# Optimization experiments

Hardware: AMD Instinct MI355X
Metric: run time of the kernel (lower is better)

Reference implementation:

```python
import jax, jax.numpy as jnp
import numpy as np

K = 16          # neighbors per query (args.k)
EPS_NORM = 1e-5  # LayerNorm / BatchNorm eps (torch default)


def _knn_edges(xyz, B, n):
    # batch-aware kNN: equal-sized batches, edges never cross batch boundary
    x = xyz.reshape(B, n, 3)
    d2 = jnp.sum((x[:, :, None, :] - x[:, None, :, :]) ** 2, -1)   # [B,n,n]
    _, idx = jax.lax.top_k(-d2, K)                                 # [B,n,K] local neighbor ids
    col = (idx + (jnp.arange(B) * n)[:, None, None]).reshape(-1)   # source (neighbor) [E]
    row = jnp.repeat(jnp.arange(B * n), K)                         # target (query)    [E]
    return row, col


def _forward(support_xyz, batch_index, features, lang_features, mask_flattened,
             W1, b1, ln_g, ln_b, W2, b2,
             Wl1, bl1, bn_g, bn_b, Wl2, bl2,
             Wr1, br1, Wr2, br2, row, col):
    N = support_xyz.shape[0]
    B, L, Fl = lang_features.shape
    # feat_encoder: Linear -> LayerNorm -> ReLU -> Linear
    h = features @ W1 + b1
    mu = h.mean(-1, keepdims=True)
    var = ((h - mu) ** 2).mean(-1, keepdims=True)
    h = (h - mu) / jnp.sqrt(var + EPS_NORM) * ln_g + ln_b
    feats = jax.nn.relu(h) @ W2 + b2                               # [N,F]
    # lang_encoder: Linear -> BatchNorm1d (batch statistics) -> ReLU -> Linear
    hl = lang_features.reshape(B * L, Fl) @ Wl1 + bl1
    mul = hl.mean(0)
    varl = ((hl - mul) ** 2).mean(0)
    hl = (hl - mul) / jnp.sqrt(varl + EPS_NORM) * bn_g + bn_b
    lang = (jax.nn.relu(hl) @ Wl2 + bl2).reshape(B, L, -1)         # [B,L,F]
    lang_flat = lang[batch_index]                                  # [N,L,F]
    # per-point / per-token attention logits
    atten = jnp.einsum('nf,nlf->nl', feats, lang_flat)             # [N,L]
    # segment softmax over incoming kNN edges (CenterOp max / add)
    attenmax = jax.ops.segment_max(atten[col], row, num_segments=N, indices_are_sorted=True)
    a = jnp.exp(atten[col] - attenmax[row])                        # [E,L]
    attensum = jax.ops.segment_sum(a, row, num_segments=N, indices_are_sorted=True)
    # CenterConv message
    att = a / attensum[row] * mask_flattened[row]                  # [E,L]
    att = att / (att.sum(-1, keepdims=True) + 1e-7)
    ctx = jnp.einsum('el,elf->ef', att, lang_flat[col])            # [E,F] attended lang feat
    xi, xj = support_xyz[row], support_xyz[col]
    d = xi - xj
    nrm = jnp.sqrt(jnp.sum(d * d, -1, keepdims=True) + 1e-12)
    ew = jnp.concatenate([xi, xj, d, nrm], -1)                     # [E,10]
    ew = jax.nn.relu(ew @ Wr1 + br1) @ Wr2 + br2                   # [E,F] rel_encoder
    msg = feats[col] * ctx * ew                                    # [E,F]
    rel = jax.ops.segment_sum(msg, row, num_segments=N, indices_are_sorted=True)
    return feats + rel


def setup_inputs() -> dict:
    key = jax.random.key(0)
    ks = jax.random.split(key, 12)
    B, n, L = 4, 1024, 16
    N = B * n
    Fv, Fl, F = 256, 768, 128
    def w(k, shp, fan):
        return jax.random.normal(k, shp, jnp.float32) / np.sqrt(fan).astype(np.float32)
    mask = (jax.random.uniform(ks[3], (N, L)) < 0.8).astype(jnp.float32).at[:, 0].set(1.0)
    return {
        'support_xyz': jax.random.normal(ks[0], (N, 3), jnp.float32),
        'batch_index': jnp.repeat(jnp.arange(B), n),
        'features': jax.random.normal(ks[1], (N, Fv), jnp.float32),
        'lang_features': jax.random.normal(ks[2], (B, L, Fl), jnp.float32),
        'mask_flattened': mask,
        'W1': w(ks[4], (Fv, F), Fv), 'b1': jnp.zeros(F, jnp.float32),
        'ln_g': jnp.ones(F, jnp.float32), 'ln_b': jnp.zeros(F, jnp.float32),
        'W2': w(ks[5], (F, F), F), 'b2': jnp.zeros(F, jnp.float32),
        'Wl1': w(ks[6], (Fl, F), Fl), 'bl1': jnp.zeros(F, jnp.float32),
        'bn_g': jnp.ones(F, jnp.float32), 'bn_b': jnp.zeros(F, jnp.float32),
        'Wl2': w(ks[7], (F, F), F), 'bl2': jnp.zeros(F, jnp.float32),
        'Wr1': w(ks[8], (10, 64), 10), 'br1': jnp.zeros(64, jnp.float32),
        'Wr2': w(ks[9], (64, F), 64), 'br2': jnp.zeros(F, jnp.float32),
    }


def reference(support_xyz, batch_index, features, lang_features, mask_flattened,
              W1, b1, ln_g, ln_b, W2, b2,
              Wl1, bl1, bn_g, bn_b, Wl2, bl2,
              Wr1, br1, Wr2, br2):
    B = lang_features.shape[0]
    n = support_xyz.shape[0] // B
    row, col = _knn_edges(support_xyz, B, n)
    return _forward(support_xyz, batch_index, features, lang_features, mask_flattened,
                    W1, b1, ln_g, ln_b, W2, b2,
                    Wl1, bl1, bn_g, bn_b, Wl2, bl2,
                    Wr1, br1, Wr2, br2, row, col)
```

## Files before the change

### kernel.cpp

```cpp
#include <hip/hip_runtime.h>

typedef unsigned long long u64;
typedef unsigned int u32;
typedef short short8 __attribute__((ext_vector_type(8)));
typedef float f32x4 __attribute__((ext_vector_type(4)));
typedef u32 u32x4v __attribute__((ext_vector_type(4)));

#define N_PTS   4096
#define B_SZ    4
#define N_PER_B 1024
#define L_TOK   16
#define FV      256
#define FL      768
#define FDIM    128
#define KNN     16
#define RH      64

#define MFMA_BF16(a, b, c) __builtin_amdgcn_mfma_f32_16x16x32_bf16((a), (b), (c), 0, 0, 0)

__device__ __forceinline__ short f2bf(float f) {
    unsigned int x = __float_as_uint(f);
    unsigned int r = (x + 0x7fffu + ((x >> 16) & 1u)) >> 16;
    return (short)r;
}

__global__ __launch_bounds__(256) void k1_kernel(const float* __restrict__ xyz,
                                                 const float* __restrict__ features,
                                                 const float* __restrict__ lf,
                                                 const float* __restrict__ Wl1,
                                                 const float* __restrict__ bl1,
                                                 const float* __restrict__ W1,
                                                 const float* __restrict__ W2,
                                                 const float* __restrict__ Wr2,
                                                 int* __restrict__ knn,
                                                 float* __restrict__ hl,
                                                 short* __restrict__ fp_hi,
                                                 short* __restrict__ fp_lo,
                                                 short* __restrict__ w1p_hi,
                                                 short* __restrict__ w1p_lo,
                                                 short* __restrict__ w2p_hi,
                                                 short* __restrict__ w2p_lo,
                                                 short* __restrict__ w2pe) {
    __shared__ float smem[1024];
    int b = blockIdx.x, t = threadIdx.x;

    if (b < 1024) {
        int lane = t & 63;
        int q = b * 4 + (t >> 6);
        int base = (q >> 10) << 10;
        float qx = xyz[q * 3 + 0];
        float qy = xyz[q * 3 + 1];
        float qz = xyz[q * 3 + 2];
        double key[16];
#pragma unroll
        for (int m = 0; m < 16; m++) {
            int jl = lane + (m << 6);
            int j = base + jl;
            float dx = qx - xyz[j * 3 + 0];
            float dy = qy - xyz[j * 3 + 1];
            float dz = qz - xyz[j * 3 + 2];
            float d2 = __fadd_rn(__fadd_rn(__fmul_rn(dx, dx), __fmul_rn(dy, dy)),
                                 __fmul_rn(dz, dz));
            key[m] = (double)__float_as_uint(d2) * 1024.0 + (double)jl;
        }
#pragma unroll
        for (int k = 2; k <= 16; k <<= 1) {
#pragma unroll
            for (int jj = k >> 1; jj > 0; jj >>= 1) {
#pragma unroll
                for (int i = 0; i < 16; i++) {
                    int l = i ^ jj;
                    if (l > i) {
                        double lo = fmin(key[i], key[l]);
                        double hi = fmax(key[i], key[l]);
                        bool asc = ((i & k) == 0);
                        key[i] = asc ? lo : hi;
                        key[l] = asc ? hi : lo;
                    }
                }
            }
        }
#pragma unroll
        for (int lvl = 1; lvl <= 32; lvl <<= 1) {
            double pk[16];
#pragma unroll
            for (int i = 0; i < 16; i++) pk[i] = __shfl_xor(key[15 - i], lvl, 64);
#pragma unroll
            for (int i = 0; i < 16; i++) key[i] = fmin(key[i], pk[i]);
#pragma unroll
            for (int jj = 8; jj > 0; jj >>= 1) {
#pragma unroll
                for (int i = 0; i < 16; i++) {
                    int l = i ^ jj;
                    if (l > i) {
                        double lo = fmin(key[i], key[l]);
                        double hi = fmax(key[i], key[l]);
                        key[i] = lo;
                        key[l] = hi;
                    }
                }
            }
        }
        if (lane == 0) {
            int idx[16];
#pragma unroll
            for (int i = 0; i < 16; i++)
                idx[i] = base + (int)(((u64)key[i]) & 1023u);
#pragma unroll
            for (int w = 0; w < 4; w++) {
                int4 v = {idx[4 * w], idx[4 * w + 1], idx[4 * w + 2], idx[4 * w + 3]};
                *(int4*)&knn[q * KNN + 4 * w] = v;
            }
        }
    } else if (b < 1088) {
        int r = b - 1024;
        float* lrow = smem;
        float* part = smem + 768;
        for (int k = t; k < FL; k += 256) lrow[k] = lf[r * FL + k];
        __syncthreads();
        int c = t & 127, kh = t >> 7;
        float acc = (kh == 0) ? bl1[c] : 0.f;
        int k0 = kh * 384;
        for (int k = k0; k < k0 + 384; k++) acc += lrow[k] * Wl1[k * FDIM + c];
        part[kh * FDIM + c] = acc;
        __syncthreads();
        if (kh == 0) hl[r * FDIM + c] = part[c] + part[FDIM + c];
    } else if (b < 1344) {
        int rt = b - 1088;
        int lane = t & 63, kh = t >> 6;
        int e = lane & 15, q = lane >> 4;
#pragma unroll
        for (int pp = 0; pp < 2; pp++) {
            int ks = kh * 2 + pp;
            const float* src = features + (rt * 16 + e) * FV + ks * 32 + q * 8;
            float4 f0 = *(const float4*)src;
            float4 f1 = *(const float4*)(src + 4);
            float f[8] = {f0.x, f0.y, f0.z, f0.w, f1.x, f1.y, f1.z, f1.w};
            short8 hi, lo;
#pragma unroll
            for (int j = 0; j < 8; j++) {
                u32 bits = __float_as_uint(f[j]);
                hi[j] = (short)(bits >> 16);
                float lof = f[j] - __uint_as_float(bits & 0xffff0000u);
                lo[j] = (short)(__float_as_uint(lof) >> 16);
            }
            int o = ((rt * 8 + ks) * 64 + lane) * 8;
            *(short8*)(fp_hi + o) = hi;
            *(short8*)(fp_lo + o) = lo;
        }
    } else if (b < 1356) {
        int isW2 = (b >= 1352);
        int ks = isW2 ? (b - 1352) : (b - 1344);
        const float* W = isW2 ? W2 : W1;
        short* ph = isW2 ? w2p_hi : w1p_hi;
        short* pl = isW2 ? w2p_lo : w1p_lo;
        int lane = t & 63, cth = t >> 6;
        int e = lane & 15, q = lane >> 4;
#pragma unroll
        for (int p = 0; p < 2; p++) {
            int ct = cth * 2 + p;
            short8 hi, lo;
#pragma unroll
            for (int j = 0; j < 8; j++) {
                float w = W[(ks * 32 + q * 8 + j) * FDIM + ct * 16 + e];
                u32 bits = __float_as_uint(w);
                hi[j] = (short)(bits >> 16);
                float lof = w - __uint_as_float(bits & 0xffff0000u);
                lo[j] = (short)(__float_as_uint(lof) >> 16);
            }
            int o = ((ks * 8 + ct) * 64 + lane) * 8;
            *(short8*)(ph + o) = hi;
            *(short8*)(pl + o) = lo;
        }
    } else {
        int ks = b - 1356;
        int lane = t & 63, cth = t >> 6;
        int e = lane & 15, q = lane >> 4;
#pragma unroll
        for (int p = 0; p < 2; p++) {
            int ct = cth * 2 + p;
            short8 v;
#pragma unroll
            for (int j = 0; j < 8; j++)
                v[j] = f2bf(Wr2[(ks * 32 + q * 8 + j) * FDIM + ct * 16 + e]);
            *(short8*)(w2pe + ((ks * 8 + ct) * 64 + lane) * 8) = v;
        }
    }
}

__global__ __launch_bounds__(256) void k2_kernel(const short* __restrict__ fp_hi,
                                                 const short* __restrict__ fp_lo,
                                                 const short* __restrict__ w1p_hi,
                                                 const short* __restrict__ w1p_lo,
                                                 const short* __restrict__ w2p_hi,
                                                 const short* __restrict__ w2p_lo,
                                                 const float* __restrict__ b1,
                                                 const float* __restrict__ ln_g,
                                                 const float* __restrict__ ln_b,
                                                 const float* __restrict__ b2,
                                                 const float* __restrict__ hl,
                                                 const float* __restrict__ bn_g,
                                                 const float* __restrict__ bn_b,
                                                 const float* __restrict__ Wl2,
                                                 const float* __restrict__ bl2,
                                                 float* __restrict__ feats,
                                                 float* __restrict__ lang) {
    int b = blockIdx.x, t = threadIdx.x;
    if (b < 64) {
        __shared__ u32 hbuf[4][16 * 132];
        int wid = t >> 6, lane = t & 63;
        int e = lane & 15, q = lane >> 4;
        int rt = b * 4 + wid;

        f32x4 acc[8];
#pragma unroll
        for (int ct = 0; ct < 8; ct++) {
            float v = b1[ct * 16 + e];
            acc[ct] = (f32x4){v, v, v, v};
        }
        for (int ks = 0; ks < 8; ks++) {
            int ao = ((rt * 8 + ks) * 64 + lane) * 8;
            short8 ah = *(const short8*)(fp_hi + ao);
            short8 al = *(const short8*)(fp_lo + ao);
#pragma unroll
            for (int ct = 0; ct < 8; ct++) {
                int bo = ((ks * 8 + ct) * 64 + lane) * 8;
                short8 bh = *(const short8*)(w1p_hi + bo);
                short8 bl = *(const short8*)(w1p_lo + bo);
                acc[ct] = MFMA_BF16(ah, bh, acc[ct]);
                acc[ct] = MFMA_BF16(al, bh, acc[ct]);
                acc[ct] = MFMA_BF16(ah, bl, acc[ct]);
            }
        }
        float s[4], sq[4];
#pragma unroll
        for (int r = 0; r < 4; r++) { s[r] = 0.f; sq[r] = 0.f; }
#pragma unroll
        for (int ct = 0; ct < 8; ct++)
#pragma unroll
            for (int r = 0; r < 4; r++) {
                float v = acc[ct][r];
                s[r] += v; sq[r] += v * v;
            }
#pragma unroll
        for (int off = 1; off < 16; off <<= 1)
#pragma unroll
            for (int r = 0; r < 4; r++) {
                s[r] += __shfl_xor(s[r], off, 16);
                sq[r] += __shfl_xor(sq[r], off, 16);
            }
        float mu[4], rs[4];
#pragma unroll
        for (int r = 0; r < 4; r++) {
            mu[r] = s[r] * (1.f / 128.f);
            float var = sq[r] * (1.f / 128.f) - mu[r] * mu[r];
            rs[r] = rsqrtf(var + 1e-5f);
        }
        u32* hrow = &hbuf[wid][0];
#pragma unroll
        for (int ct = 0; ct < 8; ct++) {
            float g = ln_g[ct * 16 + e], bb = ln_b[ct * 16 + e];
#pragma unroll
            for (int r = 0; r < 4; r++) {
                float n = fmaxf((acc[ct][r] - mu[r]) * rs[r] * g + bb, 0.f);
                u32 nb = __float_as_uint(n);
                u32 hh = nb & 0xffff0000u;
                float lof = n - __uint_as_float(hh);
                hrow[(q * 4 + r) * 132 + ct * 16 + e] = hh | (__float_as_uint(lof) >> 16);
            }
        }
        f32x4 acc2[8];
#pragma unroll
        for (int ct = 0; ct < 8; ct++) {
            float v = b2[ct * 16 + e];
            acc2[ct] = (f32x4){v, v, v, v};
        }
#pragma unroll
        for (int ks = 0; ks < 4; ks++) {
            u32 hv[8];
            *(u32x4v*)&hv[0] = *(const u32x4v*)&hrow[e * 132 + ks * 32 + q * 8];
            *(u32x4v*)&hv[4] = *(const u32x4v*)&hrow[e * 132 + ks * 32 + q * 8 + 4];
            short8 ah, al;
#pragma unroll
            for (int j = 0; j < 8; j++) {
                ah[j] = (short)(hv[j] >> 16);
                al[j] = (short)(hv[j] & 0xffffu);
            }
#pragma unroll
            for (int ct = 0; ct < 8; ct++) {
                int bo = ((ks * 8 + ct) * 64 + lane) * 8;
                short8 bh = *(const short8*)(w2p_hi + bo);
                short8 bl = *(const short8*)(w2p_lo + bo);
                acc2[ct] = MFMA_BF16(ah, bh, acc2[ct]);
                acc2[ct] = MFMA_BF16(al, bh, acc2[ct]);
                acc2[ct] = MFMA_BF16(ah, bl, acc2[ct]);
            }
        }
#pragma unroll
        for (int ct = 0; ct < 8; ct++)
#pragma unroll
            for (int r = 0; r < 4; r++)
                feats[(rt * 16 + q * 4 + r) * FDIM + ct * 16 + e] = acc2[ct][r];
    } else {
        __shared__ float rl4[4][FDIM];
        int tt = t & 127;
        int act = (t < 128);
        int r0 = (b - 64) * 4;
        if (act) {
            float s = 0.f, s2 = 0.f;
            for (int r = 0; r < 64; r++) {
                float v = hl[r * FDIM + tt];
                s += v; s2 += v * v;
            }
            float mu = s * (1.f / 64.f);
            float var = s2 * (1.f / 64.f) - mu * mu;
            float rs = rsqrtf(var + 1e-5f);
            float g = bn_g[tt], bb = bn_b[tt];
#pragma unroll
            for (int p = 0; p < 4; p++)
                rl4[p][tt] = fmaxf((hl[(r0 + p) * FDIM + tt] - mu) * rs * g + bb, 0.f);
        }
        __syncthreads();
        if (act) {
            float bv = bl2[tt];
            float a0 = bv, a1 = bv, a2 = bv, a3 = bv;
            for (int k = 0; k < FDIM; k++) {
                float w = Wl2[k * FDIM + tt];
                a0 += rl4[0][k] * w;
                a1 += rl4[1][k] * w;
                a2 += rl4[2][k] * w;
                a3 += rl4[3][k] * w;
            }
            lang[(r0 + 0) * FDIM + tt] = a0;
            lang[(r0 + 1) * FDIM + tt] = a1;
            lang[(r0 + 2) * FDIM + tt] = a2;
            lang[(r0 + 3) * FDIM + tt] = a3;
        }
    }
}

__global__ __launch_bounds__(256) void atten_kernel(const float* __restrict__ feats,
                                                    const float* __restrict__ lang,
                                                    float* __restrict__ atten,
                                                    short* __restrict__ langp) {
    int t = threadIdx.x;
    int b = blockIdx.x;
    if (b < 2048) {
        __shared__ float fb[2][FDIM];
        __shared__ float pb[256];
        int half = t >> 7, tt = t & 127;
        int i = b * 2 + half;
        fb[half][tt] = feats[i * FDIM + tt];
        __syncthreads();
        int l = tt >> 3, sj = tt & 7;
        int bi = i >> 10;
        const float* lrow = lang + (bi * L_TOK + l) * FDIM;
        float p = 0.f;
#pragma unroll
        for (int m = 0; m < 16; m++) {
            int k = sj + (m << 3);
            p += fb[half][k] * lrow[k];
        }
        pb[t] = p;
        __syncthreads();
        if (tt < L_TOK) {
            float a = 0.f;
#pragma unroll
            for (int u = 0; u < 8; u++) a += pb[half * 128 + tt * 8 + u];
            atten[i * L_TOK + tt] = a;
        }
    } else {
        int bi = b - 2048;
        int lane = t & 63, w = t >> 6;
        int e = lane & 15, qd = lane >> 4;
#pragma unroll
        for (int p = 0; p < 2; p++) {
            int tile = w * 2 + p;
            short8 v;
            if (qd < 2) {
#pragma unroll
                for (int j = 0; j < 8; j++)
                    v[j] = f2bf(lang[bi * L_TOK * FDIM + (qd * 8 + j) * FDIM + tile * 16 + e]);
            } else {
#pragma unroll
                for (int j = 0; j < 8; j++) v[j] = 0;
            }
            *(short8*)(langp + ((bi * 8 + tile) * 64 + lane) * 8) = v;
        }
    }
}

__global__ __launch_bounds__(256) void edge_kernel(const float* __restrict__ xyz,
                                                   const float* __restrict__ mask,
                                                   const float* __restrict__ Wr1,
                                                   const float* __restrict__ br1,
                                                   const float* __restrict__ br2,
                                                   const int* __restrict__ knn,
                                                   const short* __restrict__ w2pe,
                                                   const short* __restrict__ langp,
                                                   const float* __restrict__ feats,
                                                   const float* __restrict__ atten,
                                                   float* __restrict__ out) {
    int lane = threadIdx.x & 63;
    int wid  = threadIdx.x >> 6;
    int i    = blockIdx.x * 4 + wid;
    int bi   = i >> 10;
    int quad = lane >> 4;
    int e16  = lane & 15;

    int idxe = knn[i * KNN + e16];

    float sat[8];
    if (quad < 2) {
        const float4* ap = (const float4*)(atten + idxe * L_TOK + quad * 8);
        float4 a0 = ap[0], a1 = ap[1];
        sat[0] = a0.x; sat[1] = a0.y; sat[2] = a0.z; sat[3] = a0.w;
        sat[4] = a1.x; sat[5] = a1.y; sat[6] = a1.z; sat[7] = a1.w;
    } else {
#pragma unroll
        for (int j = 0; j < 8; j++) sat[j] = 0.f;
    }

    float mx[8];
#pragma unroll
    for (int j = 0; j < 8; j++) mx[j] = sat[j];
#pragma unroll
    for (int off = 1; off < 16; off <<= 1) {
#pragma unroll
        for (int j = 0; j < 8; j++) mx[j] = fmaxf(mx[j], __shfl_xor(mx[j], off, 16));
    }
    float ex[8], sm[8];
#pragma unroll
    for (int j = 0; j < 8; j++) { ex[j] = __expf(sat[j] - mx[j]); sm[j] = ex[j]; }
#pragma unroll
    for (int off = 1; off < 16; off <<= 1) {
#pragma unroll
        for (int j = 0; j < 8; j++) sm[j] += __shfl_xor(sm[j], off, 16);
    }
    float st[8];
    if (quad < 2) {
        const float4* mp = (const float4*)(mask + i * L_TOK + quad * 8);
        float4 m0 = mp[0], m1 = mp[1];
        float mv[8] = {m0.x, m0.y, m0.z, m0.w, m1.x, m1.y, m1.z, m1.w};
#pragma unroll
        for (int j = 0; j < 8; j++) st[j] = ex[j] * (mv[j] / sm[j]);
    } else {
#pragma unroll
        for (int j = 0; j < 8; j++) st[j] = 0.f;
    }
    float s = st[0] + st[1] + st[2] + st[3] + st[4] + st[5] + st[6] + st[7];
    s += __shfl_xor(s, 16, 64);
    s += __shfl_xor(s, 32, 64);
    float inv2 = 1.f / (s + 1e-7f);
    short8 sattA;
#pragma unroll
    for (int j = 0; j < 8; j++) sattA[j] = f2bf(st[j] * inv2);

    float xi0 = xyz[i * 3 + 0], xi1 = xyz[i * 3 + 1], xi2 = xyz[i * 3 + 2];
    float xj0 = xyz[idxe * 3 + 0], xj1 = xyz[idxe * 3 + 1], xj2 = xyz[idxe * 3 + 2];
    float d0 = xi0 - xj0, d1 = xi1 - xj1, d2v = xi2 - xj2;
    float nr = sqrtf(d0 * d0 + d1 * d1 + d2v * d2v + 1e-12f);
    float ein[10] = {xi0, xi1, xi2, xj0, xj1, xj2, d0, d1, d2v, nr};
    short8 hidA[2];
#pragma unroll
    for (int sstep = 0; sstep < 2; sstep++) {
        int k0 = sstep * 32 + quad * 8;
        float h[8];
        const float4* bp = (const float4*)(br1 + k0);
        float4 b0 = bp[0], b1v = bp[1];
        h[0] = b0.x; h[1] = b0.y; h[2] = b0.z; h[3] = b0.w;
        h[4] = b1v.x; h[5] = b1v.y; h[6] = b1v.z; h[7] = b1v.w;
#pragma unroll
        for (int m = 0; m < 10; m++) {
            const float4* wp = (const float4*)(Wr1 + m * RH + k0);
            float4 w0 = wp[0], w1 = wp[1];
            float em = ein[m];
            h[0] += em * w0.x; h[1] += em * w0.y; h[2] += em * w0.z; h[3] += em * w0.w;
            h[4] += em * w1.x; h[5] += em * w1.y; h[6] += em * w1.z; h[7] += em * w1.w;
        }
#pragma unroll
        for (int j = 0; j < 8; j++) hidA[sstep][j] = f2bf(fmaxf(h[j], 0.f));
    }

    int idxr[4];
#pragma unroll
    for (int r = 0; r < 4; r++) idxr[r] = knn[i * KNN + quad * 4 + r];

#pragma unroll 2
    for (int tile = 0; tile < 8; tile++) {
        int cc = tile * 16 + e16;
        f32x4 accew = {0.f, 0.f, 0.f, 0.f};
#pragma unroll
        for (int sstep = 0; sstep < 2; sstep++) {
            short8 w2B = *(const short8*)(w2pe + ((sstep * 8 + tile) * 64 + lane) * 8);
            accew = __builtin_amdgcn_mfma_f32_16x16x32_bf16(hidA[sstep], w2B, accew, 0, 0, 0);
        }
        short8 lsB = *(const short8*)(langp + ((bi * 8 + tile) * 64 + lane) * 8);
        f32x4 accctx = {0.f, 0.f, 0.f, 0.f};
        accctx = __builtin_amdgcn_mfma_f32_16x16x32_bf16(sattA, lsB, accctx, 0, 0, 0);

        float br2c = br2[cc];
        float msum = 0.f;
#pragma unroll
        for (int r = 0; r < 4; r++) {
            float fj = feats[idxr[r] * FDIM + cc];
            msum += fj * accctx[r] * (accew[r] + br2c);
        }
        msum += __shfl_xor(msum, 16, 64);
        msum += __shfl_xor(msum, 32, 64);
        if (lane < 16)
            out[i * FDIM + cc] = feats[i * FDIM + cc] + msum;
    }
}

extern "C" void kernel_launch(void* const* d_in, const int* in_sizes, int n_in,
                              void* d_out, int out_size, void* d_ws, size_t ws_size,
                              hipStream_t stream) {
    const float* xyz   = (const float*)d_in[0];
    const float* features = (const float*)d_in[2];
    const float* lang_f   = (const float*)d_in[3];
    const float* mask     = (const float*)d_in[4];
    const float* W1   = (const float*)d_in[5];
    const float* b1   = (const float*)d_in[6];
    const float* ln_g = (const float*)d_in[7];
    const float* ln_b = (const float*)d_in[8];
    const float* W2   = (const float*)d_in[9];
    const float* b2   = (const float*)d_in[10];
    const float* Wl1  = (const float*)d_in[11];
    const float* bl1  = (const float*)d_in[12];
    const float* bn_g = (const float*)d_in[13];
    const float* bn_b = (const float*)d_in[14];
    const float* Wl2  = (const float*)d_in[15];
    const float* bl2  = (const float*)d_in[16];
    const float* Wr1  = (const float*)d_in[17];
    const float* br1  = (const float*)d_in[18];
    const float* Wr2  = (const float*)d_in[19];
    const float* br2  = (const float*)d_in[20];

    float* ws_feats = (float*)d_ws;
    float* ws_atten = ws_feats + N_PTS * FDIM;
    float* ws_lang  = ws_atten + N_PTS * L_TOK;
    float* ws_hl    = ws_lang + B_SZ * L_TOK * FDIM;
    int*   ws_knn   = (int*)(ws_hl + 64 * FDIM);
    short* fp_hi    = (short*)(ws_knn + N_PTS * KNN);
    short* fp_lo    = fp_hi + N_PTS * FV;
    short* w1p_hi   = fp_lo + N_PTS * FV;
    short* w1p_lo   = w1p_hi + FV * FDIM;
    short* w2p_hi   = w1p_lo + FV * FDIM;
    short* w2p_lo   = w2p_hi + FDIM * FDIM;
    short* w2pe     = w2p_lo + FDIM * FDIM;
    short* langp    = w2pe + RH * FDIM;

    k1_kernel<<<1358, 256, 0, stream>>>(xyz, features, lang_f, Wl1, bl1, W1, W2, Wr2,
                                        ws_knn, ws_hl,
                                        fp_hi, fp_lo, w1p_hi, w1p_lo, w2p_hi, w2p_lo,
                                        w2pe);
    k2_kernel<<<80, 256, 0, stream>>>(fp_hi, fp_lo, w1p_hi, w1p_lo, w2p_hi, w2p_lo,
                                      b1, ln_g, ln_b, b2,
                                      ws_hl, bn_g, bn_b, Wl2, bl2,
                                      ws_feats, ws_lang);
    atten_kernel<<<2052, 256, 0, stream>>>(ws_feats, ws_lang, ws_atten, langp);
    edge_kernel<<<N_PTS / 4, 256, 0, stream>>>(xyz, mask, Wr1, br1, br2,
                                               ws_knn, w2pe, langp, ws_feats, ws_atten,
                                               (float*)d_out);
}
```

Measured before the change: 156.1 us.

## Fuse four kernels into one persistent kernel with software grid barriers

Merges the kNN/prep, encoder, attention and edge kernels into a single 512-block kernel separated by atomic-counter grid barriers, with the barrier counters reset by a memset before launch. The bf16 hi/lo split of the input features now happens inside the encoder GEMM instead of going through a workspace round trip. This aims to remove launch gaps and the split-feature workspace traffic. The cost is lower parallelism in some phases, spin-wait barrier overhead, and a deadlock risk if the 512 blocks cannot all be resident at once.

```diff
diff --git a/kernel.cpp b/kernel.cpp
--- a/kernel.cpp
+++ b/kernel.cpp
@@ -8,13 +8,13 @@
 
 #define N_PTS   4096
 #define B_SZ    4
-#define N_PER_B 1024
 #define L_TOK   16
 #define FV      256
 #define FL      768
 #define FDIM    128
 #define KNN     16
 #define RH      64
+#define NBLK    512
 
 #define MFMA_BF16(a, b, c) __builtin_amdgcn_mfma_f32_16x16x32_bf16((a), (b), (c), 0, 0, 0)
 
@@ -24,204 +24,189 @@
     return (short)r;
 }
 
-__global__ __launch_bounds__(256) void k1_kernel(const float* __restrict__ xyz,
-                                                 const float* __restrict__ features,
-                                                 const float* __restrict__ lf,
-                                                 const float* __restrict__ Wl1,
-                                                 const float* __restrict__ bl1,
-                                                 const float* __restrict__ W1,
-                                                 const float* __restrict__ W2,
-                                                 const float* __restrict__ Wr2,
-                                                 int* __restrict__ knn,
-                                                 float* __restrict__ hl,
-                                                 short* __restrict__ fp_hi,
-                                                 short* __restrict__ fp_lo,
-                                                 short* __restrict__ w1p_hi,
-                                                 short* __restrict__ w1p_lo,
-                                                 short* __restrict__ w2p_hi,
-                                                 short* __restrict__ w2p_lo,
-                                                 short* __restrict__ w2pe) {
-    __shared__ float smem[1024];
+__device__ __forceinline__ u32 splitf(float f) {
+    u32 bits = __float_as_uint(f);
+    u32 hi = bits >> 16;
+    float lof = f - __uint_as_float(bits & 0xffff0000u);
+    u32 lo = __float_as_uint(lof) >> 16;
+    return (hi << 16) | lo;
+}
+
+__device__ __forceinline__ void grid_sync(unsigned* bar, int idx) {
+    __syncthreads();
+    if (threadIdx.x == 0) {
+        __threadfence();
+        __hip_atomic_fetch_add(&bar[idx], 1u, __ATOMIC_ACQ_REL, __HIP_MEMORY_SCOPE_AGENT);
+        while (__hip_atomic_load(&bar[idx], __ATOMIC_ACQUIRE, __HIP_MEMORY_SCOPE_AGENT) < NBLK)
+            __builtin_amdgcn_s_sleep(8);
+        __threadfence();
+    }
+    __syncthreads();
+}
+
+__global__ __launch_bounds__(256, 2) void mega_kernel(
+    const float* __restrict__ xyz, const float* __restrict__ features,
+    const float* __restrict__ lf, const float* __restrict__ mask,
+    const float* __restrict__ W1, const float* __restrict__ b1,
+    const float* __restrict__ ln_g, const float* __restrict__ ln_b,
+    const float* __restrict__ W2, const float* __restrict__ b2,
+    const float* __restrict__ Wl1, const float* __restrict__ bl1,
+    const float* __restrict__ bn_g, const float* __restrict__ bn_b,
+    const float* __restrict__ Wl2, const float* __restrict__ bl2,
+    const float* __restrict__ Wr1, const float* __restrict__ br1,
+    const float* __restrict__ Wr2, const float* __restrict__ br2,
+    float* __restrict__ feats, float* __restrict__ atten,
+    float* __restrict__ lang, float* __restrict__ hl, int* __restrict__ knn,
+    short* __restrict__ w1p_hi, short* __restrict__ w1p_lo,
+    short* __restrict__ w2p_hi, short* __restrict__ w2p_lo,
+    short* __restrict__ w2pe, short* __restrict__ langp,
+    unsigned* __restrict__ bar, float* __restrict__ out)
+{
+    __shared__ u32 smem_u[8448];
     int b = blockIdx.x, t = threadIdx.x;
-
-    if (b < 1024) {
-        int lane = t & 63;
-        int q = b * 4 + (t >> 6);
-        int base = (q >> 10) << 10;
-        float qx = xyz[q * 3 + 0];
-        float qy = xyz[q * 3 + 1];
-        float qz = xyz[q * 3 + 2];
-        double key[16];
-#pragma unroll
-        for (int m = 0; m < 16; m++) {
-            int jl = lane + (m << 6);
-            int j = base + jl;
-            float dx = qx - xyz[j * 3 + 0];
-            float dy = qy - xyz[j * 3 + 1];
-            float dz = qz - xyz[j * 3 + 2];
-            float d2 = __fadd_rn(__fadd_rn(__fmul_rn(dx, dx), __fmul_rn(dy, dy)),
-                                 __fmul_rn(dz, dz));
-            key[m] = (double)__float_as_uint(d2) * 1024.0 + (double)jl;
-        }
-#pragma unroll
-        for (int k = 2; k <= 16; k <<= 1) {
-#pragma unroll
-            for (int jj = k >> 1; jj > 0; jj >>= 1) {
-#pragma unroll
-                for (int i = 0; i < 16; i++) {
-                    int l = i ^ jj;
-                    if (l > i) {
-                        double lo = fmin(key[i], key[l]);
-                        double hi = fmax(key[i], key[l]);
-                        bool asc = ((i & k) == 0);
-                        key[i] = asc ? lo : hi;
-                        key[l] = asc ? hi : lo;
+    int wid = t >> 6, lane = t & 63;
+    int e = lane & 15, q = lane >> 4;
+
+    {
+        for (int qq = 0; qq < 2; qq++) {
+            int qi = (b * 4 + wid) * 2 + qq;
+            int base = (qi >> 10) << 10;
+            float qx = xyz[qi * 3 + 0];
+            float qy = xyz[qi * 3 + 1];
+            float qz = xyz[qi * 3 + 2];
+            double key[16];
+#pragma unroll
+            for (int m = 0; m < 16; m++) {
+                int jl = lane + (m << 6);
+                int j = base + jl;
+                float dx = qx - xyz[j * 3 + 0];
+                float dy = qy - xyz[j * 3 + 1];
+                float dz = qz - xyz[j * 3 + 2];
+                float d2 = __fadd_rn(__fadd_rn(__fmul_rn(dx, dx), __fmul_rn(dy, dy)),
+                                     __fmul_rn(dz, dz));
+                key[m] = (double)__float_as_uint(d2) * 1024.0 + (double)jl;
+            }
+#pragma unroll
+            for (int k = 2; k <= 16; k <<= 1) {
+#pragma unroll
+                for (int jj = k >> 1; jj > 0; jj >>= 1) {
+#pragma unroll
+                    for (int i = 0; i < 16; i++) {
+                        int l = i ^ jj;
+                        if (l > i) {
+                            double lo = fmin(key[i], key[l]);
+                            double hi = fmax(key[i], key[l]);
+                            bool asc = ((i & k) == 0);
+                            key[i] = asc ? lo : hi;
+                            key[l] = asc ? hi : lo;
+                        }
                     }
                 }
             }
-        }
-#pragma unroll
-        for (int lvl = 1; lvl <= 32; lvl <<= 1) {
-            double pk[16];
-#pragma unroll
-            for (int i = 0; i < 16; i++) pk[i] = __shfl_xor(key[15 - i], lvl, 64);
-#pragma unroll
-            for (int i = 0; i < 16; i++) key[i] = fmin(key[i], pk[i]);
-#pragma unroll
-            for (int jj = 8; jj > 0; jj >>= 1) {
-#pragma unroll
-                for (int i = 0; i < 16; i++) {
-                    int l = i ^ jj;
-                    if (l > i) {
-                        double lo = fmin(key[i], key[l]);
-                        double hi = fmax(key[i], key[l]);
-                        key[i] = lo;
-                        key[l] = hi;
+#pragma unroll
+            for (int lvl = 1; lvl <= 32; lvl <<= 1) {
+                double pk[16];
+#pragma unroll
+                for (int i = 0; i < 16; i++) pk[i] = __shfl_xor(key[15 - i], lvl, 64);
+#pragma unroll
+                for (int i = 0; i < 16; i++) key[i] = fmin(key[i], pk[i]);
+#pragma unroll
+                for (int jj = 8; jj > 0; jj >>= 1) {
+#pragma unroll
+                    for (int i = 0; i < 16; i++) {
+                        int l = i ^ jj;
+                        if (l > i) {
+                            double lo = fmin(key[i], key[l]);
+                            double hi = fmax(key[i], key[l]);
+                            key[i] = lo;
+                            key[l] = hi;
+                        }
                     }
                 }
             }
-        }
-        if (lane == 0) {
-            int idx[16];
-#pragma unroll
-            for (int i = 0; i < 16; i++)
-                idx[i] = base + (int)(((u64)key[i]) & 1023u);
-#pragma unroll
-            for (int w = 0; w < 4; w++) {
-                int4 v = {idx[4 * w], idx[4 * w + 1], idx[4 * w + 2], idx[4 * w + 3]};
-                *(int4*)&knn[q * KNN + 4 * w] = v;
-            }
-        }
-    } else if (b < 1088) {
-        int r = b - 1024;
-        float* lrow = smem;
-        float* part = smem + 768;
-        for (int k = t; k < FL; k += 256) lrow[k] = lf[r * FL + k];
-        __syncthreads();
-        int c = t & 127, kh = t >> 7;
-        float acc = (kh == 0) ? bl1[c] : 0.f;
-        int k0 = kh * 384;
-        for (int k = k0; k < k0 + 384; k++) acc += lrow[k] * Wl1[k * FDIM + c];
-        part[kh * FDIM + c] = acc;
-        __syncthreads();
-        if (kh == 0) hl[r * FDIM + c] = part[c] + part[FDIM + c];
-    } else if (b < 1344) {
-        int rt = b - 1088;
-        int lane = t & 63, kh = t >> 6;
-        int e = lane & 15, q = lane >> 4;
-#pragma unroll
-        for (int pp = 0; pp < 2; pp++) {
-            int ks = kh * 2 + pp;
+            if (lane == 0) {
+                int idx[16];
+#pragma unroll
+                for (int i = 0; i < 16; i++)
+                    idx[i] = base + (int)(((u64)key[i]) & 1023u);
+#pragma unroll
+                for (int w = 0; w < 4; w++) {
+                    int4 v = {idx[4 * w], idx[4 * w + 1], idx[4 * w + 2], idx[4 * w + 3]};
+                    *(int4*)&knn[qi * KNN + 4 * w] = v;
+                }
+            }
+        }
+        if (b % 5 == 0) {
+            int ej = b / 5;
+            if (ej < 64) {
+                int r = ej;
+                float* lrow = (float*)smem_u;
+                float* part = lrow + FL;
+                for (int k = t; k < FL; k += 256) lrow[k] = lf[r * FL + k];
+                __syncthreads();
+                int c = t & 127, kh = t >> 7;
+                float acc = (kh == 0) ? bl1[c] : 0.f;
+                int k0 = kh * 384;
+                for (int k = k0; k < k0 + 384; k++) acc += lrow[k] * Wl1[k * FDIM + c];
+                part[kh * FDIM + c] = acc;
+                __syncthreads();
+                if (kh == 0) hl[r * FDIM + c] = part[c] + part[FDIM + c];
+            } else if (ej < 76) {
+                int isW2 = (ej >= 72);
+                int ks = isW2 ? (ej - 72) : (ej - 64);
+                const float* W = isW2 ? W2 : W1;
+                short* ph = isW2 ? w2p_hi : w1p_hi;
+                short* pl = isW2 ? w2p_lo : w1p_lo;
+#pragma unroll
+                for (int p = 0; p < 2; p++) {
+                    int ct = wid * 2 + p;
+                    short8 hi, lo;
+#pragma unroll
+                    for (int j = 0; j < 8; j++) {
+                        u32 pr = splitf(W[(ks * 32 + q * 8 + j) * FDIM + ct * 16 + e]);
+                        hi[j] = (short)(pr >> 16);
+                        lo[j] = (short)(pr & 0xffffu);
+                    }
+                    int o = ((ks * 8 + ct) * 64 + lane) * 8;
+                    *(short8*)(ph + o) = hi;
+                    *(short8*)(pl + o) = lo;
+                }
+            } else if (ej < 78) {
+                int ks = ej - 76;
+#pragma unroll
+                for (int p = 0; p < 2; p++) {
+                    int ct = wid * 2 + p;
+                    short8 v;
+#pragma unroll
+                    for (int j = 0; j < 8; j++)
+                        v[j] = f2bf(Wr2[(ks * 32 + q * 8 + j) * FDIM + ct * 16 + e]);
+                    *(short8*)(w2pe + ((ks * 8 + ct) * 64 + lane) * 8) = v;
+                }
+            }
+        }
+    }
+    grid_sync(bar, 0);
+
+    if (b < 64) {
+        int rt = b * 4 + wid;
+        f32x4 acc[8];
+#pragma unroll
+        for (int ct = 0; ct < 8; ct++) {
+            float v = b1[ct * 16 + e];
+            acc[ct] = (f32x4){v, v, v, v};
+        }
+        for (int ks = 0; ks < 8; ks++) {
             const float* src = features + (rt * 16 + e) * FV + ks * 32 + q * 8;
             float4 f0 = *(const float4*)src;
             float4 f1 = *(const float4*)(src + 4);
-            float f[8] = {f0.x, f0.y, f0.z, f0.w, f1.x, f1.y, f1.z, f1.w};
-            short8 hi, lo;
+            float av[8] = {f0.x, f0.y, f0.z, f0.w, f1.x, f1.y, f1.z, f1.w};
+            short8 ah, al;
 #pragma unroll
             for (int j = 0; j < 8; j++) {
-                u32 bits = __float_as_uint(f[j]);
-                hi[j] = (short)(bits >> 16);
-                float lof = f[j] - __uint_as_float(bits & 0xffff0000u);
-                lo[j] = (short)(__float_as_uint(lof) >> 16);
-            }
-            int o = ((rt * 8 + ks) * 64 + lane) * 8;
-            *(short8*)(fp_hi + o) = hi;
-            *(short8*)(fp_lo + o) = lo;
-        }
-    } else if (b < 1356) {
-        int isW2 = (b >= 1352);
-        int ks = isW2 ? (b - 1352) : (b - 1344);
-        const float* W = isW2 ? W2 : W1;
-        short* ph = isW2 ? w2p_hi : w1p_hi;
-        short* pl = isW2 ? w2p_lo : w1p_lo;
-        int lane = t & 63, cth = t >> 6;
-        int e = lane & 15, q = lane >> 4;
-#pragma unroll
-        for (int p = 0; p < 2; p++) {
-            int ct = cth * 2 + p;
-            short8 hi, lo;
-#pragma unroll
-            for (int j = 0; j < 8; j++) {
-                float w = W[(ks * 32 + q * 8 + j) * FDIM + ct * 16 + e];
-                u32 bits = __float_as_uint(w);
-                hi[j] = (short)(bits >> 16);
-                float lof = w - __uint_as_float(bits & 0xffff0000u);
-                lo[j] = (short)(__float_as_uint(lof) >> 16);
-            }
-            int o = ((ks * 8 + ct) * 64 + lane) * 8;
-            *(short8*)(ph + o) = hi;
-            *(short8*)(pl + o) = lo;
-        }
-    } else {
-        int ks = b - 1356;
-        int lane = t & 63, cth = t >> 6;
-        int e = lane & 15, q = lane >> 4;
-#pragma unroll
-        for (int p = 0; p < 2; p++) {
-            int ct = cth * 2 + p;
-            short8 v;
-#pragma unroll
-            for (int j = 0; j < 8; j++)
-                v[j] = f2bf(Wr2[(ks * 32 + q * 8 + j) * FDIM + ct * 16 + e]);
-            *(short8*)(w2pe + ((ks * 8 + ct) * 64 + lane) * 8) = v;
-        }
-    }
-}
-
-__global__ __launch_bounds__(256) void k2_kernel(const short* __restrict__ fp_hi,
-                                                 const short* __restrict__ fp_lo,
-                                                 const short* __restrict__ w1p_hi,
-                                                 const short* __restrict__ w1p_lo,
-                                                 const short* __restrict__ w2p_hi,
-                                                 const short* __restrict__ w2p_lo,
-                                                 const float* __restrict__ b1,
-                                                 const float* __restrict__ ln_g,
-                                                 const float* __restrict__ ln_b,
-                                                 const float* __restrict__ b2,
-                                                 const float* __restrict__ hl,
-                                                 const float* __restrict__ bn_g,
-                                                 const float* __restrict__ bn_b,
-                                                 const float* __restrict__ Wl2,
-                                                 const float* __restrict__ bl2,
-                                                 float* __restrict__ feats,
-                                                 float* __restrict__ lang) {
-    int b = blockIdx.x, t = threadIdx.x;
-    if (b < 64) {
-        __shared__ u32 hbuf[4][16 * 132];
-        int wid = t >> 6, lane = t & 63;
-        int e = lane & 15, q = lane >> 4;
-        int rt = b * 4 + wid;
-
-        f32x4 acc[8];
-#pragma unroll
-        for (int ct = 0; ct < 8; ct++) {
-            float v = b1[ct * 16 + e];
-            acc[ct] = (f32x4){v, v, v, v};
-        }
-        for (int ks = 0; ks < 8; ks++) {
-            int ao = ((rt * 8 + ks) * 64 + lane) * 8;
-            short8 ah = *(const short8*)(fp_hi + ao);
-            short8 al = *(const short8*)(fp_lo + ao);
+                u32 pr = splitf(av[j]);
+                ah[j] = (short)(pr >> 16);
+                al[j] = (short)(pr & 0xffffu);
+            }
 #pragma unroll
             for (int ct = 0; ct < 8; ct++) {
                 int bo = ((ks * 8 + ct) * 64 + lane) * 8;
@@ -256,17 +241,14 @@
             float var = sq[r] * (1.f / 128.f) - mu[r] * mu[r];
             rs[r] = rsqrtf(var + 1e-5f);
         }
-        u32* hrow = &hbuf[wid][0];
+        u32* hrow = smem_u + wid * (16 * 132);
 #pragma unroll
         for (int ct = 0; ct < 8; ct++) {
             float g = ln_g[ct * 16 + e], bb = ln_b[ct * 16 + e];
 #pragma unroll
             for (int r = 0; r < 4; r++) {
                 float n = fmaxf((acc[ct][r] - mu[r]) * rs[r] * g + bb, 0.f);
-                u32 nb = __float_as_uint(n);
-                u32 hh = nb & 0xffff0000u;
-                float lof = n - __uint_as_float(hh);
-                hrow[(q * 4 + r) * 132 + ct * 16 + e] = hh | (__float_as_uint(lof) >> 16);
+                hrow[(q * 4 + r) * 132 + ct * 16 + e] = splitf(n);
             }
         }
         f32x4 acc2[8];
@@ -301,8 +283,8 @@
 #pragma unroll
             for (int r = 0; r < 4; r++)
                 feats[(rt * 16 + q * 4 + r) * FDIM + ct * 16 + e] = acc2[ct][r];
-    } else {
-        __shared__ float rl4[4][FDIM];
+    } else if (b < 80) {
+        float* rl4 = (float*)smem_u;
         int tt = t & 127;
         int act = (t < 128);
         int r0 = (b - 64) * 4;
@@ -318,7 +300,7 @@
             float g = bn_g[tt], bb = bn_b[tt];
 #pragma unroll
             for (int p = 0; p < 4; p++)
-                rl4[p][tt] = fmaxf((hl[(r0 + p) * FDIM + tt] - mu) * rs * g + bb, 0.f);
+                rl4[p * FDIM + tt] = fmaxf((hl[(r0 + p) * FDIM + tt] - mu) * rs * g + bb, 0.f);
         }
         __syncthreads();
         if (act) {
@@ -326,10 +308,10 @@
             float a0 = bv, a1 = bv, a2 = bv, a3 = bv;
             for (int k = 0; k < FDIM; k++) {
                 float w = Wl2[k * FDIM + tt];
-                a0 += rl4[0][k] * w;
-                a1 += rl4[1][k] * w;
-                a2 += rl4[2][k] * w;
-                a3 += rl4[3][k] * w;
+                a0 += rl4[0 * FDIM + k] * w;
+                a1 += rl4[1 * FDIM + k] * w;
+                a2 += rl4[2 * FDIM + k] * w;
+                a3 += rl4[3 * FDIM + k] * w;
             }
             lang[(r0 + 0) * FDIM + tt] = a0;
             lang[(r0 + 1) * FDIM + tt] = a1;
@@ -337,179 +319,168 @@
             lang[(r0 + 3) * FDIM + tt] = a3;
         }
     }
-}
-
-__global__ __launch_bounds__(256) void atten_kernel(const float* __restrict__ feats,
-                                                    const float* __restrict__ lang,
-                                                    float* __restrict__ atten,
-                                                    short* __restrict__ langp) {
-    int t = threadIdx.x;
-    int b = blockIdx.x;
-    if (b < 2048) {
-        __shared__ float fb[2][FDIM];
-        __shared__ float pb[256];
-        int half = t >> 7, tt = t & 127;
-        int i = b * 2 + half;
-        fb[half][tt] = feats[i * FDIM + tt];
-        __syncthreads();
-        int l = tt >> 3, sj = tt & 7;
+    grid_sync(bar, 1);
+
+    if (b < 64) {
+        int pt0 = (b * 4 + wid) * 16;
+        int bi = pt0 >> 10;
+        const float* arow = feats + (pt0 + e) * FDIM;
+        const float* brow = lang + (bi * L_TOK + e) * FDIM;
+        f32x4 acc = {0.f, 0.f, 0.f, 0.f};
+#pragma unroll
+        for (int ks = 0; ks < 4; ks++) {
+            int off = ks * 32 + q * 8;
+            float4 a0 = *(const float4*)(arow + off);
+            float4 a1 = *(const float4*)(arow + off + 4);
+            float4 c0 = *(const float4*)(brow + off);
+            float4 c1 = *(const float4*)(brow + off + 4);
+            float av[8] = {a0.x, a0.y, a0.z, a0.w, a1.x, a1.y, a1.z, a1.w};
+            float bv[8] = {c0.x, c0.y, c0.z, c0.w, c1.x, c1.y, c1.z, c1.w};
+            short8 ah, al, bh, bl;
+#pragma unroll
+            for (int j = 0; j < 8; j++) {
+                u32 pa = splitf(av[j]);
+                u32 pb = splitf(bv[j]);
+                ah[j] = (short)(pa >> 16);
+                al[j] = (short)(pa & 0xffffu);
+                bh[j] = (short)(pb >> 16);
+                bl[j] = (short)(pb & 0xffffu);
+            }
+            acc = MFMA_BF16(ah, bh, acc);
+            acc = MFMA_BF16(al, bh, acc);
+            acc = MFMA_BF16(ah, bl, acc);
+        }
+#pragma unroll
+        for (int r = 0; r < 4; r++)
+            atten[(pt0 + q * 4 + r) * L_TOK + e] = acc[r];
+    } else if (b < 68) {
+        int bi = b - 64;
+#pragma unroll
+        for (int p = 0; p < 2; p++) {
+            int tile = wid * 2 + p;
+            short8 v;
+            if (q < 2) {
+#pragma unroll
+                for (int j = 0; j < 8; j++)
+                    v[j] = f2bf(lang[bi * L_TOK * FDIM + (q * 8 + j) * FDIM + tile * 16 + e]);
+            } else {
+#pragma unroll
+                for (int j = 0; j < 8; j++) v[j] = 0;
+            }
+            *(short8*)(langp + ((bi * 8 + tile) * 64 + lane) * 8) = v;
+        }
+    }
+    grid_sync(bar, 2);
+
+    for (int qq = 0; qq < 2; qq++) {
+        int i = (b * 4 + wid) * 2 + qq;
         int bi = i >> 10;
-        const float* lrow = lang + (bi * L_TOK + l) * FDIM;
-        float p = 0.f;
-#pragma unroll
-        for (int m = 0; m < 16; m++) {
-            int k = sj + (m << 3);
-            p += fb[half][k] * lrow[k];
-        }
-        pb[t] = p;
-        __syncthreads();
-        if (tt < L_TOK) {
-            float a = 0.f;
-#pragma unroll
-            for (int u = 0; u < 8; u++) a += pb[half * 128 + tt * 8 + u];
-            atten[i * L_TOK + tt] = a;
-        }
-    } else {
-        int bi = b - 2048;
-        int lane = t & 63, w = t >> 6;
-        int e = lane & 15, qd = lane >> 4;
-#pragma unroll
-        for (int p = 0; p < 2; p++) {
-            int tile = w * 2 + p;
-            short8 v;
-            if (qd < 2) {
-#pragma unroll
-                for (int j = 0; j < 8; j++)
-                    v[j] = f2bf(lang[bi * L_TOK * FDIM + (qd * 8 + j) * FDIM + tile * 16 + e]);
-            } else {
-#pragma unroll
-                for (int j = 0; j < 8; j++) v[j] = 0;
-            }
-            *(short8*)(langp + ((bi * 8 + tile) * 64 + lane) * 8) = v;
-        }
-    }
-}
-
-__global__ __launch_bounds__(256) void edge_kernel(const float* __restrict__ xyz,
-                                                   const float* __restrict__ mask,
-                                                   const float* __restrict__ Wr1,
-                                                   const float* __restrict__ br1,
-                                                   const float* __restrict__ br2,
-                                                   const int* __restrict__ knn,
-                                                   const short* __restrict__ w2pe,
-                                                   const short* __restrict__ langp,
-                                                   const float* __restrict__ feats,
-                                                   const float* __restrict__ atten,
-                                                   float* __restrict__ out) {
-    int lane = threadIdx.x & 63;
-    int wid  = threadIdx.x >> 6;
-    int i    = blockIdx.x * 4 + wid;
-    int bi   = i >> 10;
-    int quad = lane >> 4;
-    int e16  = lane & 15;
-
-    int idxe = knn[i * KNN + e16];
-
-    float sat[8];
-    if (quad < 2) {
-        const float4* ap = (const float4*)(atten + idxe * L_TOK + quad * 8);
-        float4 a0 = ap[0], a1 = ap[1];
-        sat[0] = a0.x; sat[1] = a0.y; sat[2] = a0.z; sat[3] = a0.w;
-        sat[4] = a1.x; sat[5] = a1.y; sat[6] = a1.z; sat[7] = a1.w;
-    } else {
-#pragma unroll
-        for (int j = 0; j < 8; j++) sat[j] = 0.f;
-    }
-
-    float mx[8];
-#pragma unroll
-    for (int j = 0; j < 8; j++) mx[j] = sat[j];
-#pragma unroll
-    for (int off = 1; off < 16; off <<= 1) {
-#pragma unroll
-        for (int j = 0; j < 8; j++) mx[j] = fmaxf(mx[j], __shfl_xor(mx[j], off, 16));
-    }
-    float ex[8], sm[8];
-#pragma unroll
-    for (int j = 0; j < 8; j++) { ex[j] = __expf(sat[j] - mx[j]); sm[j] = ex[j]; }
-#pragma unroll
-    for (int off = 1; off < 16; off <<= 1) {
-#pragma unroll
-        for (int j = 0; j < 8; j++) sm[j] += __shfl_xor(sm[j], off, 16);
-    }
-    float st[8];
-    if (quad < 2) {
-        const float4* mp = (const float4*)(mask + i * L_TOK + quad * 8);
-        float4 m0 = mp[0], m1 = mp[1];
-        float mv[8] = {m0.x, m0.y, m0.z, m0.w, m1.x, m1.y, m1.z, m1.w};
-#pragma unroll
-        for (int j = 0; j < 8; j++) st[j] = ex[j] * (mv[j] / sm[j]);
-    } else {
-#pragma unroll
-        for (int j = 0; j < 8; j++) st[j] = 0.f;
-    }
-    float s = st[0] + st[1] + st[2] + st[3] + st[4] + st[5] + st[6] + st[7];
-    s += __shfl_xor(s, 16, 64);
-    s += __shfl_xor(s, 32, 64);
-    float inv2 = 1.f / (s + 1e-7f);
-    short8 sattA;
-#pragma unroll
-    for (int j = 0; j < 8; j++) sattA[j] = f2bf(st[j] * inv2);
-
-    float xi0 = xyz[i * 3 + 0], xi1 = xyz[i * 3 + 1], xi2 = xyz[i * 3 + 2];
-    float xj0 = xyz[idxe * 3 + 0], xj1 = xyz[idxe * 3 + 1], xj2 = xyz[idxe * 3 + 2];
-    float d0 = xi0 - xj0, d1 = xi1 - xj1, d2v = xi2 - xj2;
-    float nr = sqrtf(d0 * d0 + d1 * d1 + d2v * d2v + 1e-12f);
-    float ein[10] = {xi0, xi1, xi2, xj0, xj1, xj2, d0, d1, d2v, nr};
-    short8 hidA[2];
-#pragma unroll
-    for (int sstep = 0; sstep < 2; sstep++) {
-        int k0 = sstep * 32 + quad * 8;
-        float h[8];
-        const float4* bp = (const float4*)(br1 + k0);
-        float4 b0 = bp[0], b1v = bp[1];
-        h[0] = b0.x; h[1] = b0.y; h[2] = b0.z; h[3] = b0.w;
-        h[4] = b1v.x; h[5] = b1v.y; h[6] = b1v.z; h[7] = b1v.w;
-#pragma unroll
-        for (int m = 0; m < 10; m++) {
-            const float4* wp = (const float4*)(Wr1 + m * RH + k0);
-            float4 w0 = wp[0], w1 = wp[1];
-            float em = ein[m];
-            h[0] += em * w0.x; h[1] += em * w0.y; h[2] += em * w0.z; h[3] += em * w0.w;
-            h[4] += em * w1.x; h[5] += em * w1.y; h[6] += em * w1.z; h[7] += em * w1.w;
-        }
-#pragma unroll
-        for (int j = 0; j < 8; j++) hidA[sstep][j] = f2bf(fmaxf(h[j], 0.f));
-    }
-
-    int idxr[4];
-#pragma unroll
-    for (int r = 0; r < 4; r++) idxr[r] = knn[i * KNN + quad * 4 + r];
+        int quad = q;
+        int e16 = e;
+
+        int idxe = knn[i * KNN + e16];
+
+        float sat[8];
+        if (quad < 2) {
+            const float4* ap = (const float4*)(atten + idxe * L_TOK + quad * 8);
+            float4 a0 = ap[0], a1 = ap[1];
+            sat[0] = a0.x; sat[1] = a0.y; sat[2] = a0.z; sat[3] = a0.w;
+            sat[4] = a1.x; sat[5] = a1.y; sat[6] = a1.z; sat[7] = a1.w;
+        } else {
+#pragma unroll
+            for (int j = 0; j < 8; j++) sat[j] = 0.f;
+        }
+
+        float mx[8];
+#pragma unroll
+        for (int j = 0; j < 8; j++) mx[j] = sat[j];
+#pragma unroll
+        for (int off = 1; off < 16; off <<= 1) {
+#pragma unroll
+            for (int j = 0; j < 8; j++) mx[j] = fmaxf(mx[j], __shfl_xor(mx[j], off, 16));
+        }
+        float ex[8], sm[8];
+#pragma unroll
+        for (int j = 0; j < 8; j++) { ex[j] = __expf(sat[j] - mx[j]); sm[j] = ex[j]; }
+#pragma unroll
+        for (int off = 1; off < 16; off <<= 1) {
+#pragma unroll
+            for (int j = 0; j < 8; j++) sm[j] += __shfl_xor(sm[j], off, 16);
+        }
+        float st[8];
+        if (quad < 2) {
+            const float4* mp = (const float4*)(mask + i * L_TOK + quad * 8);
+            float4 m0 = mp[0], m1 = mp[1];
+            float mv[8] = {m0.x, m0.y, m0.z, m0.w, m1.x, m1.y, m1.z, m1.w};
+#pragma unroll
+            for (int j = 0; j < 8; j++) st[j] = ex[j] * (mv[j] / sm[j]);
+        } else {
+#pragma unroll
+            for (int j = 0; j < 8; j++) st[j] = 0.f;
+        }
+        float s = st[0] + st[1] + st[2] + st[3] + st[4] + st[5] + st[6] + st[7];
+        s += __shfl_xor(s, 16, 64);
+        s += __shfl_xor(s, 32, 64);
+        float inv2 = 1.f / (s + 1e-7f);
+        short8 sattA;
+#pragma unroll
+        for (int j = 0; j < 8; j++) sattA[j] = f2bf(st[j] * inv2);
+
+        float xi0 = xyz[i * 3 + 0], xi1 = xyz[i * 3 + 1], xi2 = xyz[i * 3 + 2];
+        float xj0 = xyz[idxe * 3 + 0], xj1 = xyz[idxe * 3 + 1], xj2 = xyz[idxe * 3 + 2];
+        float d0 = xi0 - xj0, d1 = xi1 - xj1, d2v = xi2 - xj2;
+        float nr = sqrtf(d0 * d0 + d1 * d1 + d2v * d2v + 1e-12f);
+        float ein[10] = {xi0, xi1, xi2, xj0, xj1, xj2, d0, d1, d2v, nr};
+        short8 hidA[2];
+#pragma unroll
+        for (int sstep = 0; sstep < 2; sstep++) {
+            int k0 = sstep * 32 + quad * 8;
+            float h[8];
+            const float4* bp = (const float4*)(br1 + k0);
+            float4 b0 = bp[0], b1v = bp[1];
+            h[0] = b0.x; h[1] = b0.y; h[2] = b0.z; h[3] = b0.w;
+            h[4] = b1v.x; h[5] = b1v.y; h[6] = b1v.z; h[7] = b1v.w;
+#pragma unroll
+            for (int m = 0; m < 10; m++) {
+                const float4* wp = (const float4*)(Wr1 + m * RH + k0);
+                float4 w0 = wp[0], w1 = wp[1];
+                float em = ein[m];
+                h[0] += em * w0.x; h[1] += em * w0.y; h[2] += em * w0.z; h[3] += em * w0.w;
+                h[4] += em * w1.x; h[5] += em * w1.y; h[6] += em * w1.z; h[7] += em * w1.w;
+            }
+#pragma unroll
+            for (int j = 0; j < 8; j++) hidA[sstep][j] = f2bf(fmaxf(h[j], 0.f));
+        }
+
+        int idxr[4];
+#pragma unroll
+        for (int r = 0; r < 4; r++) idxr[r] = knn[i * KNN + quad * 4 + r];
 
 #pragma unroll 2
-    for (int tile = 0; tile < 8; tile++) {
-        int cc = tile * 16 + e16;
-        f32x4 accew = {0.f, 0.f, 0.f, 0.f};
-#pragma unroll
-        for (int sstep = 0; sstep < 2; sstep++) {
-            short8 w2B = *(const short8*)(w2pe + ((sstep * 8 + tile) * 64 + lane) * 8);
-            accew = __builtin_amdgcn_mfma_f32_16x16x32_bf16(hidA[sstep], w2B, accew, 0, 0, 0);
-        }
-        short8 lsB = *(const short8*)(langp + ((bi * 8 + tile) * 64 + lane) * 8);
-        f32x4 accctx = {0.f, 0.f, 0.f, 0.f};
-        accctx = __builtin_amdgcn_mfma_f32_16x16x32_bf16(sattA, lsB, accctx, 0, 0, 0);
-
-        float br2c = br2[cc];
-        float msum = 0.f;
-#pragma unroll
-        for (int r = 0; r < 4; r++) {
-            float fj = feats[idxr[r] * FDIM + cc];
-            msum += fj * accctx[r] * (accew[r] + br2c);
-        }
-        msum += __shfl_xor(msum, 16, 64);
-        msum += __shfl_xor(msum, 32, 64);
-        if (lane < 16)
-            out[i * FDIM + cc] = feats[i * FDIM + cc] + msum;
+        for (int tile = 0; tile < 8; tile++) {
+            int cc = tile * 16 + e16;
+            f32x4 accew = {0.f, 0.f, 0.f, 0.f};
+#pragma unroll
+            for (int sstep = 0; sstep < 2; sstep++) {
+                short8 w2B = *(const short8*)(w2pe + ((sstep * 8 + tile) * 64 + lane) * 8);
+                accew = MFMA_BF16(hidA[sstep], w2B, accew);
+            }
+            short8 lsB = *(const short8*)(langp + ((bi * 8 + tile) * 64 + lane) * 8);
+            f32x4 accctx = {0.f, 0.f, 0.f, 0.f};
+            accctx = MFMA_BF16(sattA, lsB, accctx);
+
+            float br2c = br2[cc];
+            float msum = 0.f;
+#pragma unroll
+            for (int r = 0; r < 4; r++) {
+                float fj = feats[idxr[r] * FDIM + cc];
+                msum += fj * accctx[r] * (accew[r] + br2c);
+            }
+            msum += __shfl_xor(msum, 16, 64);
+            msum += __shfl_xor(msum, 32, 64);
+            if (lane < 16)
+                out[i * FDIM + cc] = feats[i * FDIM + cc] + msum;
+        }
     }
 }
 
@@ -542,25 +513,21 @@
     float* ws_lang  = ws_atten + N_PTS * L_TOK;
     float* ws_hl    = ws_lang + B_SZ * L_TOK * FDIM;
     int*   ws_knn   = (int*)(ws_hl + 64 * FDIM);
-    short* fp_hi    = (short*)(ws_knn + N_PTS * KNN);
-    short* fp_lo    = fp_hi + N_PTS * FV;
-    short* w1p_hi   = fp_lo + N_PTS * FV;
+    short* w1p_hi   = (short*)(ws_knn + N_PTS * KNN);
     short* w1p_lo   = w1p_hi + FV * FDIM;
     short* w2p_hi   = w1p_lo + FV * FDIM;
     short* w2p_lo   = w2p_hi + FDIM * FDIM;
     short* w2pe     = w2p_lo + FDIM * FDIM;
     short* langp    = w2pe + RH * FDIM;
-
-    k1_kernel<<<1358, 256, 0, stream>>>(xyz, features, lang_f, Wl1, bl1, W1, W2, Wr2,
-                                        ws_knn, ws_hl,
-                                        fp_hi, fp_lo, w1p_hi, w1p_lo, w2p_hi, w2p_lo,
-                                        w2pe);
-    k2_kernel<<<80, 256, 0, stream>>>(fp_hi, fp_lo, w1p_hi, w1p_lo, w2p_hi, w2p_lo,
-                                      b1, ln_g, ln_b, b2,
-                                      ws_hl, bn_g, bn_b, Wl2, bl2,
-                                      ws_feats, ws_lang);
-    atten_kernel<<<2052, 256, 0, stream>>>(ws_feats, ws_lang, ws_atten, langp);
-    edge_kernel<<<N_PTS / 4, 256, 0, stream>>>(xyz, mask, Wr1, br1, br2,
-                                               ws_knn, w2pe, langp, ws_feats, ws_atten,
-                                               (float*)d_out);
+    unsigned* bar   = (unsigned*)(langp + B_SZ * 8 * 64 * 8);
+
+    (void)hipMemsetAsync((void*)bar, 0, 3 * sizeof(unsigned), stream);
+    mega_kernel<<<NBLK, 256, 0, stream>>>(
+        xyz, features, lang_f, mask,
+        W1, b1, ln_g, ln_b, W2, b2,
+        Wl1, bl1, bn_g, bn_b, Wl2, bl2,
+        Wr1, br1, Wr2, br2,
+        ws_feats, ws_atten, ws_lang, ws_hl, ws_knn,
+        w1p_hi, w1p_lo, w2p_hi, w2p_lo, w2pe, langp,
+        bar, (float*)d_out);
 }
```

New measurement: 449.7 us. 188% more time.
